# Performance work log

Hardware: AMD Instinct MI355X
Metric: run time of the kernel (lower is better)

The kernel has to match this reference:

```python
import jax, jax.numpy as jnp
import numpy as np

BS9 = 9
NA9 = BS9 * BS9  # 81


def _make_windows():
    """All 5-in-a-row windows on a 9x9 board, as flat cell indices. (140, 5)."""
    wins = []
    for dr, dc in ((0, 1), (1, 0), (1, 1), (1, -1)):
        for r in range(BS9):
            for c in range(BS9):
                er, ec = r + 4 * dr, c + 4 * dc
                if 0 <= er < BS9 and 0 <= ec < BS9:
                    wins.append([(r + k * dr) * BS9 + (c + k * dc) for k in range(5)])
    return np.asarray(wins, dtype=np.int32)

_W_NP = _make_windows()                      # (140, 5)
_M_NP = np.zeros((NA9, _W_NP.shape[0]), dtype=np.int32)
for w in range(_W_NP.shape[0]):
    _M_NP[_W_NP[w], w] = 1                   # MEMBER[idx, w] = 1 iff cell idx is in window w

WINDOWS = jnp.asarray(_W_NP)                 # (140, 5)
MEMBER = jnp.asarray(_M_NP)                  # (81, 140)
# score table indexed by stone count 0..5 (pc>=5 clamps to 5 since window len is 5)
TABLE = jnp.asarray([0.0, 5.0, 50.0, 500.0, 5000.0, 100000.0], dtype=jnp.float32)


def setup_inputs() -> dict:
    key = jax.random.key(0)
    k1, k2 = jax.random.split(key)
    B = 2048
    boards = jax.random.randint(k1, (B, NA9), 0, 3).astype(jnp.float32)   # cells in {0,1,2}
    current_player = jax.random.randint(k2, (B,), 1, 3).astype(jnp.int32) # {1,2}
    return {"boards": boards, "current_player": current_player}


def reference(boards, current_player):
    # boards: (B, 81) float32 with values {0,1,2}; current_player: (B,) int32 {1,2}
    player = current_player.astype(boards.dtype)[:, None, None]  # (B,1,1)
    opp = 3.0 - player
    cells = boards[:, WINDOWS]                                    # (B,140,5)
    pc = jnp.sum(cells == player, axis=-1)                        # (B,140) player count per window
    oc = jnp.sum(cells == opp, axis=-1)                           # (B,140) opponent count

    # static eval of the current board (used for the value head)
    plus = jnp.where((oc == 0) & (pc > 0), TABLE[pc], 0.0)
    minus = jnp.where((pc == 0) & (oc > 0), TABLE[oc], 0.0)
    ev = jnp.sum(plus - minus, axis=-1)                           # (B,)

    # 1-ply lookahead: placing player's stone at empty cell idx adds MEMBER[idx] to pc
    pc_new = pc[:, None, :] + MEMBER[None]                        # (B,81,140)
    win = jnp.any((MEMBER[None] == 1) & (pc_new == 5), axis=-1)   # (B,81)
    ocb = oc[:, None, :]
    plus_n = jnp.where((ocb == 0) & (pc_new > 0), TABLE[pc_new], 0.0)
    minus_n = jnp.where((pc_new == 0) & (ocb > 0), TABLE[ocb], 0.0)
    score = jnp.sum(plus_n - minus_n, axis=-1)                    # (B,81)

    empty = boards == 0                                           # (B,81)
    logits = jnp.where(empty, jnp.where(win, 100000.0, score), -1000000.0)
    policy = jax.nn.softmax(logits * 0.03, axis=-1)               # (B,81)
    value = jnp.clip(jnp.tanh(ev / 3000.0), -0.95, 0.95)[:, None] # (B,1)
    return policy, value
```

## Files before the change

### kernel.cpp

```cpp
#include <hip/hip_runtime.h>
#include <math.h>

#define NB 81
#define NW 140

struct Tables {
    unsigned long long mlo[NW];
    unsigned long long mhi[NW];
    unsigned cw32[NB][5];
};

constexpr Tables make_tables() {
    Tables t{};
    for (int a = 0; a < NB; ++a)
        for (int j = 0; j < 5; ++j) t.cw32[a][j] = 0x8C8C8C8Cu;
    int cnt[NB] = {};
    const int DR[4] = {0, 1, 1, 1};
    const int DC[4] = {1, 0, 1, -1};
    int w = 0;
    for (int d = 0; d < 4; ++d)
        for (int r = 0; r < 9; ++r)
            for (int c = 0; c < 9; ++c) {
                const int er = r + 4 * DR[d], ec = c + 4 * DC[d];
                if (er < 0 || er > 8 || ec < 0 || ec > 8) continue;
                unsigned long long lo = 0, hi = 0;
                for (int k = 0; k < 5; ++k) {
                    const int cell = (r + k * DR[d]) * 9 + (c + k * DC[d]);
                    if (cell < 64) lo |= 1ull << cell;
                    else           hi |= 1ull << (cell - 64);
                    const int i = cnt[cell]++;
                    t.cw32[cell][i >> 2] &= ~(0xFFu << (8 * (i & 3)));
                    t.cw32[cell][i >> 2] |= (unsigned)w << (8 * (i & 3));
                }
                t.mlo[w] = lo; t.mhi[w] = hi; ++w;
            }
    return t;
}

__device__ __constant__ Tables TAB = make_tables();
__device__ __constant__ float PT[6] = {0.f, 5.f, 50.f, 500.f, 5000.f, 100000.f};
__device__ __constant__ float DT[6] = {5.f, 45.f, 450.f, 4500.f, 95000.f, 0.f};

__device__ __forceinline__ float wave_sum(float v) {
#pragma unroll
    for (int m = 1; m < 64; m <<= 1) v += __shfl_xor(v, m, 64);
    return v;
}
__device__ __forceinline__ float wave_max(float v) {
#pragma unroll
    for (int m = 1; m < 64; m <<= 1) v = fmaxf(v, __shfl_xor(v, m, 64));
    return v;
}

__global__ __launch_bounds__(256) void heur9_kernel(const float* __restrict__ boards,
                                                    const int* __restrict__ cur,
                                                    float* __restrict__ out, int B) {
    __shared__ float sD[4][NW + 1];
    const int wave = threadIdx.x >> 6;
    const int lane = threadIdx.x & 63;
    const int b = (blockIdx.x << 2) | wave;
    float* dl = sD[wave];
    const float* brd = boards + b * NB;

    const float pf = (float)cur[b];
    const float of = 3.0f - pf;
    const float v1 = brd[lane];
    const float v2 = (lane < NB - 64) ? brd[lane + 64] : -1.0f;

    const unsigned long long p_lo = __ballot(v1 == pf);
    const unsigned long long p_hi = __ballot((lane < NB - 64) && v2 == pf);
    const unsigned long long o_lo = __ballot(v1 == of);
    const unsigned long long o_hi = __ballot((lane < NB - 64) && v2 == of);
    const unsigned long long e_lo = ~(p_lo | o_lo);
    const unsigned long long e_hi = ~(p_hi | o_hi);

    float evp = 0.f;
    for (int w = lane; w < NW; w += 64) {
        const int pc = __popcll(p_lo & TAB.mlo[w]) + __popcll(p_hi & TAB.mhi[w]);
        const int oc = __popcll(o_lo & TAB.mlo[w]) + __popcll(o_hi & TAB.mhi[w]);
        float d = 0.f;
        if (oc == 0)      { d = DT[pc]; evp += PT[pc]; }
        else if (pc == 0) { d = PT[oc]; evp -= PT[oc]; }
        if (pc == 4) d = 1.0e9f;
        dl[w] = d;
    }
    if (lane == 0) dl[NW] = 0.f;
    const float ev = wave_sum(evp);
    __syncthreads();

    float sd1 = 0.f, sd2 = 0.f;
#pragma unroll
    for (int j = 0; j < 5; ++j) {
        const unsigned q = TAB.cw32[lane][j];
        sd1 += dl[q & 255] + dl[(q >> 8) & 255] + dl[(q >> 16) & 255] + dl[q >> 24];
    }
    if (lane < NB - 64) {
#pragma unroll
        for (int j = 0; j < 5; ++j) {
            const unsigned q = TAB.cw32[lane + 64][j];
            sd2 += dl[q & 255] + dl[(q >> 8) & 255] + dl[(q >> 16) & 255] + dl[q >> 24];
        }
    }
    const bool emp1 = (e_lo >> lane) & 1ull;
    const bool emp2 = (lane < NB - 64) && ((e_hi >> lane) & 1ull);
    float l1 = emp1 ? (sd1 >= 5.0e8f ? 100000.f : ev + sd1) : -1000000.f;
    float l2 = (lane < NB - 64)
                 ? (emp2 ? (sd2 >= 5.0e8f ? 100000.f : ev + sd2) : -1000000.f)
                 : -INFINITY;
    l1 *= 0.03f; l2 *= 0.03f;

    const float m = wave_max(fmaxf(l1, l2));
    const float e1 = __expf(l1 - m);
    const float e2 = (lane < NB - 64) ? __expf(l2 - m) : 0.f;
    const float inv = 1.0f / wave_sum(e1 + e2);

    out[b * NB + lane] = e1 * inv;
    if (lane < NB - 64) out[b * NB + lane + 64] = e2 * inv;
    if (lane == 0) {
        const float v = tanhf(ev * (1.f / 3000.f));
        out[B * NB + b] = fminf(fmaxf(v, -0.95f), 0.95f);
    }
}

extern "C" void kernel_launch(void* const* d_in, const int* in_sizes, int n_in,
                              void* d_out, int out_size, void* d_ws, size_t ws_size,
                              hipStream_t stream) {
    const float* boards = (const float*)d_in[0];
    const int* cur = (const int*)d_in[1];
    float* out = (float*)d_out;
    const int B = in_sizes[0] / NB;
    heur9_kernel<<<B / 4, 256, 0, stream>>>(boards, cur, out, B);
}
```

Measured before the change: 58.13 us.

## Compute window scores via per-line prefix sums and DPP wave reductions

Reorganizes the 140 windows into 36 board lines, with each lane walking up to five windows along one line. Each lane builds integer prefix sums of per-window deltas in shared memory, so each cell's lookahead score becomes a difference of two prefix entries per direction instead of summing up to 20 gathered window values. A combined (oc,pc) lookup table replaces the branching per window. Wave shuffles are replaced with DPP row operations plus readlane for the reductions. The __syncthreads is dropped in favour of an lgkmcnt wait, which relies on intra-wave ordering of LDS accesses. Integer accumulation changes float rounding slightly.

```diff
diff --git a/kernel.cpp b/kernel.cpp
--- a/kernel.cpp
+++ b/kernel.cpp
@@ -3,64 +3,151 @@
 
 #define NB 81
 #define NW 140
-
-struct Tables {
-    unsigned long long mlo[NW];
-    unsigned long long mhi[NW];
-    unsigned cw32[NB][5];
-};
-
-constexpr Tables make_tables() {
-    Tables t{};
-    for (int a = 0; a < NB; ++a)
-        for (int j = 0; j < 5; ++j) t.cw32[a][j] = 0x8C8C8C8Cu;
-    int cnt[NB] = {};
-    const int DR[4] = {0, 1, 1, 1};
-    const int DC[4] = {1, 0, 1, -1};
-    int w = 0;
-    for (int d = 0; d < 4; ++d)
-        for (int r = 0; r < 9; ++r)
-            for (int c = 0; c < 9; ++c) {
-                const int er = r + 4 * DR[d], ec = c + 4 * DC[d];
-                if (er < 0 || er > 8 || ec < 0 || ec > 8) continue;
-                unsigned long long lo = 0, hi = 0;
-                for (int k = 0; k < 5; ++k) {
-                    const int cell = (r + k * DR[d]) * 9 + (c + k * DC[d]);
-                    if (cell < 64) lo |= 1ull << cell;
-                    else           hi |= 1ull << (cell - 64);
-                    const int i = cnt[cell]++;
-                    t.cw32[cell][i >> 2] &= ~(0xFFu << (8 * (i & 3)));
-                    t.cw32[cell][i >> 2] |= (unsigned)w << (8 * (i & 3));
+#define MARK (1 << 24)
+
+
+struct LineGeom { int r0, c0, dr, dc, n; };
+constexpr LineGeom line_geom(int id) {
+    const int d = id / 9, li = id % 9;
+    if (d == 0) return LineGeom{li, 0, 0, 1, 5};
+    if (d == 1) return LineGeom{0, li, 1, 0, 5};
+    if (d == 2) {
+        const int k = li - 4;
+        const int r0 = k > 0 ? k : 0, c0 = k < 0 ? -k : 0;
+        const int L = 9 - (k < 0 ? -k : k);
+        return LineGeom{r0, c0, 1, 1, L - 4};
+    }
+    const int s = li + 4;
+    const int r0 = s > 8 ? s - 8 : 0, c0 = s - r0;
+    const int L = 9 - (s > 8 ? s - 8 : 8 - s);
+    return LineGeom{r0, c0, 1, -1, L - 4};
+}
+
+struct alignas(16) LWin { unsigned long long lo; unsigned hi; unsigned flag; };
+struct LineTab { LWin w[36][5]; };
+constexpr LineTab make_lines() {
+    LineTab t{};
+    for (int id = 0; id < 36; ++id) {
+        const LineGeom g = line_geom(id);
+        for (int k = 0; k < 5; ++k) {
+            unsigned long long lo = 0; unsigned hi = 0; unsigned flag = 48;
+            if (k < g.n) {
+                flag = 0;
+                for (int j = 0; j < 5; ++j) {
+                    const int cell = (g.r0 + (k + j) * g.dr) * 9 + (g.c0 + (k + j) * g.dc);
+                    if (cell < 64) lo |= 1ull << cell; else hi |= 1u << (cell - 64);
                 }
-                t.mlo[w] = lo; t.mhi[w] = hi; ++w;
             }
+            t.w[id][k] = LWin{lo, hi, flag};
+        }
+    }
     return t;
 }
 
-__device__ __constant__ Tables TAB = make_tables();
-__device__ __constant__ float PT[6] = {0.f, 5.f, 50.f, 500.f, 5000.f, 100000.f};
-__device__ __constant__ float DT[6] = {5.f, 45.f, 450.f, 4500.f, 95000.f, 0.f};
-
-__device__ __forceinline__ float wave_sum(float v) {
-#pragma unroll
-    for (int m = 1; m < 64; m <<= 1) v += __shfl_xor(v, m, 64);
-    return v;
-}
-__device__ __forceinline__ float wave_max(float v) {
-#pragma unroll
-    for (int m = 1; m < 64; m <<= 1) v = fmaxf(v, __shfl_xor(v, m, 64));
-    return v;
-}
+struct I2 { int d, e; };
+struct WTabI { I2 v[96]; };
+constexpr WTabI make_wt() {
+    WTabI t{};
+    int PT[6] = {0, 5, 50, 500, 5000, 100000};
+    for (int oc = 0; oc < 6; ++oc)
+        for (int pc = 0; pc < 6; ++pc) {
+            int d = 0, e = 0;
+            if (oc == 0)      { if (pc < 5) d = PT[pc + 1] - PT[pc]; e = PT[pc]; }
+            else if (pc == 0) { d = PT[oc]; e = -PT[oc]; }
+            if (pc == 4) d = MARK;
+            t.v[oc * 8 + pc] = I2{d, e};
+        }
+    return t;
+}
+
+struct CellIdx { unsigned short s[NB][8]; };
+constexpr CellIdx make_cidx() {
+    CellIdx t{};
+    for (int r = 0; r < 9; ++r)
+        for (int c = 0; c < 9; ++c) {
+            const int cell = r * 9 + c;
+            for (int d = 0; d < 4; ++d) {
+                int lo = 0, hi = 0, line = -1, i = 0;
+                if (d == 0)      { line = r;     i = c; }
+                else if (d == 1) { line = 9 + c; i = r; }
+                else if (d == 2) { const int k = r - c; if (k >= -4 && k <= 4) { line = 18 + (k + 4); i = (r < c ? r : c); } }
+                else             { const int s = r + c; if (s >= 4 && s <= 12) { line = 27 + (s - 4); i = r - (s > 8 ? s - 8 : 0); } }
+                if (line >= 0) {
+                    const LineGeom g = line_geom(line);
+                    const int jlo = (i - 4 > 0) ? i - 4 : 0;
+                    const int jhi = (i < g.n - 1) ? i : g.n - 1;
+                    lo = line * 8 + jlo;
+                    hi = line * 8 + jhi + 1;
+                }
+                t.s[cell][2 * d]     = (unsigned short)lo;
+                t.s[cell][2 * d + 1] = (unsigned short)hi;
+            }
+        }
+    return t;
+}
+
+__device__ __constant__ LineTab LT = make_lines();
+__device__ __constant__ WTabI  WT = make_wt();
+__device__ __constant__ CellIdx CIX = make_cidx();
+
+#define DPP_ADD_F(v, ctrl, rmask)                                                            \
+    v += __int_as_float(                                                                     \
+        __builtin_amdgcn_update_dpp(0, __float_as_int(v), ctrl, rmask, 0xF, true));
+#define DPP_MAX_F(v, ctrl, rmask)                                                            \
+    {                                                                                        \
+        const int _x = __builtin_amdgcn_update_dpp(__float_as_int(v), __float_as_int(v),     \
+                                                   ctrl, rmask, 0xF, false);                 \
+        v = fmaxf(v, __int_as_float(_x));                                                    \
+    }
+
+__device__ __forceinline__ float wave_red_sum(float v) {
+    DPP_ADD_F(v, 0x111, 0xF)  DPP_ADD_F(v, 0x112, 0xF)  DPP_ADD_F(v, 0x114, 0xF)
+    DPP_ADD_F(v, 0x118, 0xF)  DPP_ADD_F(v, 0x142, 0xA)  DPP_ADD_F(v, 0x143, 0xC)
+    return __int_as_float(__builtin_amdgcn_readlane(__float_as_int(v), 63));
+}
+__device__ __forceinline__ float wave_red_max(float v) {
+    DPP_MAX_F(v, 0x111, 0xF)  DPP_MAX_F(v, 0x112, 0xF)  DPP_MAX_F(v, 0x114, 0xF)
+    DPP_MAX_F(v, 0x118, 0xF)  DPP_MAX_F(v, 0x142, 0xA)  DPP_MAX_F(v, 0x143, 0xC)
+    return __int_as_float(__builtin_amdgcn_readlane(__float_as_int(v), 63));
+}
+__device__ __forceinline__ int wave_red_sum_i(int v) {
+    v += __builtin_amdgcn_update_dpp(0, v, 0x111, 0xF, 0xF, true);
+    v += __builtin_amdgcn_update_dpp(0, v, 0x112, 0xF, 0xF, true);
+    v += __builtin_amdgcn_update_dpp(0, v, 0x114, 0xF, 0xF, true);
+    v += __builtin_amdgcn_update_dpp(0, v, 0x118, 0xF, 0xF, true);
+    v += __builtin_amdgcn_update_dpp(0, v, 0x142, 0xA, 0xF, true);
+    v += __builtin_amdgcn_update_dpp(0, v, 0x143, 0xC, 0xF, true);
+    return __builtin_amdgcn_readlane(v, 63);
+}
+
+#define WSTEP(M, Cin, Cout)                                                                  \
+    {                                                                                        \
+        const unsigned long long lo = M.x | ((unsigned long long)M.y << 32);                 \
+        const int pc = __popcll(p_lo & lo) + __popc(ph & M.z);                               \
+        const int oc = __popcll(o_lo & lo) + __popc(oh & M.z);                               \
+        const I2 tt = WT.v[M.w + (oc << 3) + pc];                                            \
+        evp += tt.e;                                                                         \
+        Cout = Cin + (unsigned)tt.d;                                                         \
+    }
 
 __global__ __launch_bounds__(256) void heur9_kernel(const float* __restrict__ boards,
                                                     const int* __restrict__ cur,
                                                     float* __restrict__ out, int B) {
-    __shared__ float sD[4][NW + 1];
+    __shared__ unsigned sC[4][320];
     const int wave = threadIdx.x >> 6;
     const int lane = threadIdx.x & 63;
     const int b = (blockIdx.x << 2) | wave;
-    float* dl = sD[wave];
+    unsigned* cw = sC[wave];
     const float* brd = boards + b * NB;
+
+    const uint4 ci1 = *(const uint4*)&CIX.s[lane][0];
+    uint4 ci2 = make_uint4(0, 0, 0, 0);
+    if (lane < NB - 64) ci2 = *(const uint4*)&CIX.s[lane + 64][0];
+    uint4 lt0{}, lt1{}, lt2{}, lt3{}, lt4{};
+    if (lane < 36) {
+        const uint4* lt = (const uint4*)&LT.w[lane][0];
+        lt0 = lt[0]; lt1 = lt[1]; lt2 = lt[2]; lt3 = lt[3]; lt4 = lt[4];
+    }
 
     const float pf = (float)cur[b];
     const float of = 3.0f - pf;
@@ -68,51 +155,53 @@
     const float v2 = (lane < NB - 64) ? brd[lane + 64] : -1.0f;
 
     const unsigned long long p_lo = __ballot(v1 == pf);
-    const unsigned long long p_hi = __ballot((lane < NB - 64) && v2 == pf);
+    const unsigned long long p_hi = __ballot(v2 == pf);
     const unsigned long long o_lo = __ballot(v1 == of);
-    const unsigned long long o_hi = __ballot((lane < NB - 64) && v2 == of);
+    const unsigned long long o_hi = __ballot(v2 == of);
     const unsigned long long e_lo = ~(p_lo | o_lo);
     const unsigned long long e_hi = ~(p_hi | o_hi);
 
-    float evp = 0.f;
-    for (int w = lane; w < NW; w += 64) {
-        const int pc = __popcll(p_lo & TAB.mlo[w]) + __popcll(p_hi & TAB.mhi[w]);
-        const int oc = __popcll(o_lo & TAB.mlo[w]) + __popcll(o_hi & TAB.mhi[w]);
-        float d = 0.f;
-        if (oc == 0)      { d = DT[pc]; evp += PT[pc]; }
-        else if (pc == 0) { d = PT[oc]; evp -= PT[oc]; }
-        if (pc == 4) d = 1.0e9f;
-        dl[w] = d;
-    }
-    if (lane == 0) dl[NW] = 0.f;
-    const float ev = wave_sum(evp);
-    __syncthreads();
-
-    float sd1 = 0.f, sd2 = 0.f;
-#pragma unroll
-    for (int j = 0; j < 5; ++j) {
-        const unsigned q = TAB.cw32[lane][j];
-        sd1 += dl[q & 255] + dl[(q >> 8) & 255] + dl[(q >> 16) & 255] + dl[q >> 24];
-    }
-    if (lane < NB - 64) {
-#pragma unroll
-        for (int j = 0; j < 5; ++j) {
-            const unsigned q = TAB.cw32[lane + 64][j];
-            sd2 += dl[q & 255] + dl[(q >> 8) & 255] + dl[(q >> 16) & 255] + dl[q >> 24];
-        }
-    }
+    int evp = 0;
+    if (lane < 36) {
+        const unsigned ph = (unsigned)p_hi, oh = (unsigned)o_hi;
+        unsigned C0 = 0, C1, C2, C3, C4, C5;
+        WSTEP(lt0, C0, C1)
+        WSTEP(lt1, C1, C2)
+        WSTEP(lt2, C2, C3)
+        WSTEP(lt3, C3, C4)
+        WSTEP(lt4, C4, C5)
+        *(uint4*)(cw + lane * 8) = make_uint4(C0, C1, C2, C3);
+        *(uint2*)(cw + lane * 8 + 4) = make_uint2(C4, C5);
+    }
+    const float ev = (float)wave_red_sum_i(evp);
+
+    asm volatile("s_waitcnt lgkmcnt(0)" ::: "memory");
+
+#define RD(s) ((int)cw[(s)])
+    const int s1 = RD(ci1.x >> 16) - RD(ci1.x & 0xFFFF)
+                 + RD(ci1.y >> 16) - RD(ci1.y & 0xFFFF)
+                 + RD(ci1.z >> 16) - RD(ci1.z & 0xFFFF)
+                 + RD(ci1.w >> 16) - RD(ci1.w & 0xFFFF);
+    int s2 = 0;
+    if (lane < NB - 64)
+        s2 = RD(ci2.x >> 16) - RD(ci2.x & 0xFFFF)
+           + RD(ci2.y >> 16) - RD(ci2.y & 0xFFFF)
+           + RD(ci2.z >> 16) - RD(ci2.z & 0xFFFF)
+           + RD(ci2.w >> 16) - RD(ci2.w & 0xFFFF);
+#undef RD
+
     const bool emp1 = (e_lo >> lane) & 1ull;
     const bool emp2 = (lane < NB - 64) && ((e_hi >> lane) & 1ull);
-    float l1 = emp1 ? (sd1 >= 5.0e8f ? 100000.f : ev + sd1) : -1000000.f;
+    float l1 = emp1 ? (s1 >= MARK ? 100000.f : ev + (float)s1) : -1000000.f;
     float l2 = (lane < NB - 64)
-                 ? (emp2 ? (sd2 >= 5.0e8f ? 100000.f : ev + sd2) : -1000000.f)
+                 ? (emp2 ? (s2 >= MARK ? 100000.f : ev + (float)s2) : -1000000.f)
                  : -INFINITY;
     l1 *= 0.03f; l2 *= 0.03f;
 
-    const float m = wave_max(fmaxf(l1, l2));
+    const float m = wave_red_max(fmaxf(l1, l2));
     const float e1 = __expf(l1 - m);
     const float e2 = (lane < NB - 64) ? __expf(l2 - m) : 0.f;
-    const float inv = 1.0f / wave_sum(e1 + e2);
+    const float inv = 1.0f / wave_red_sum(e1 + e2);
 
     out[b * NB + lane] = e1 * inv;
     if (lane < NB - 64) out[b * NB + lane + 64] = e2 * inv;
```

After: 56.34 us. 3.1% less time.
